# Kernel tuning notes

Hardware: AMD Instinct MI355X
Metric: run time of the kernel (lower is better)

The kernel has to match this reference:

```python
import jax, jax.numpy as jnp
import numpy as np

K_BITS = 8
QMAX = float(2 ** (K_BITS - 1) - 1)  # 127 for symmetric int8 fake quant
BN_EPS = 1e-5
RES_SCALE = 1.0


def _ste(v, q):
    # straight-through estimator: forward q, backward identity wrt v
    return v + jax.lax.stop_gradient(q - v)


def quant_act(x, alpha):
    # PAMS-style: clamp to learnable alpha, symmetric uniform fake-quant
    xc = jnp.clip(x, -alpha, alpha)
    scale = alpha / QMAX
    q = jnp.round(xc / scale) * scale
    return _ste(xc, q)


def quant_weight(w):
    # symmetric max-abs weight fake-quant
    scale = jnp.max(jnp.abs(w)) / QMAX
    q = jnp.clip(jnp.round(w / scale), -QMAX, QMAX) * scale
    return _ste(w, q)


def conv3x3(x, w):
    return jax.lax.conv_general_dilated(
        x, w, window_strides=(1, 1), padding=[(1, 1), (1, 1)],
        dimension_numbers=("NCHW", "OIHW", "NCHW"))


def batchnorm(x, gamma, beta):
    # training-mode BN: biased batch statistics over (N, H, W)
    mean = jnp.mean(x, axis=(0, 2, 3), keepdims=True)
    var = jnp.var(x, axis=(0, 2, 3), keepdims=True)
    xhat = (x - mean) * jax.lax.rsqrt(var + BN_EPS)
    return xhat * gamma[None, :, None, None] + beta[None, :, None, None]


def prelu(x, a):
    return jnp.where(x >= 0, x, a * x)


def setup_inputs() -> dict:
    key = jax.random.key(0)
    ks = jax.random.split(key, 4)
    C = 64
    identity = jax.random.normal(ks[0], (8, C, 192, 192), dtype=jnp.float32)
    # conv weights, default_init_weights scale 0.1 (kaiming-ish * 0.1)
    w1 = jax.random.normal(ks[1], (C, C, 3, 3), dtype=jnp.float32) * 0.1
    w2 = jax.random.normal(ks[2], (C, C, 3, 3), dtype=jnp.float32) * 0.1
    return {
        "identity": identity,
        "bits": jnp.ones((1,), jnp.float32),
        "f": jnp.ones((1,), jnp.float32),
        "bits_out": jnp.zeros((1,), jnp.float32),
        "w1": w1,
        "w2": w2,
        "alpha1": jnp.array(8.0, jnp.float32),
        "alpha2": jnp.array(8.0, jnp.float32),
        "gamma1": jnp.ones((C,), jnp.float32),
        "beta1": jnp.zeros((C,), jnp.float32),
        "gamma2": jnp.ones((C,), jnp.float32),
        "beta2": jnp.zeros((C,), jnp.float32),
        "prelu_a": jnp.array(0.25, jnp.float32),
        "shortcut": jnp.ones((1,), jnp.float32),
    }


def reference(identity, bits, f, bits_out, w1, w2, alpha1, alpha2,
              gamma1, beta1, gamma2, beta2, prelu_a, shortcut):
    # quant conv1: quantize input act + weights, 3x3 conv
    x = conv3x3(quant_act(identity, alpha1), quant_weight(w1))
    # PReLU then BN1 (module applies bn1(act(x)))
    x = batchnorm(prelu(x, prelu_a), gamma1, beta1)
    # quant conv2
    out = conv3x3(quant_act(x, alpha2), quant_weight(w2))
    out = batchnorm(out, gamma2, beta2)
    out = identity * shortcut + out * RES_SCALE
    return (out, bits, f, bits_out)
```

## Files before the change

kernel.cpp:

```cpp
#include <hip/hip_runtime.h>
#include <hip/hip_bf16.h>
#include <math.h>

#define CNUM   64
#define HH     192
#define WW     192
#define NBATCH 8
#define HWSZ   (HH * WW)
#define CHWSZ  (CNUM * HWSZ)
#define TOTALSZ ((size_t)NBATCH * CHWSZ)
#define QMAXF  127.0f
#define BNEPS  1e-5f
#define PW     194

typedef __attribute__((ext_vector_type(8))) short bf16x8;
typedef __attribute__((ext_vector_type(4))) float f32x4;

#define OFF_PK1    0
#define OFF_PK2    18432
#define OFF_STATS  36864
#define OFF_SUM1   36864
#define OFF_SSQ1   37120
#define OFF_SUM2   37376
#define OFF_SSQ2   37632
#define OFF_WMAX   37888
#define OFF_SW     37890
#define OFF_QA     38148
#define OFF_QB     (38148 + 9634816)

__device__ inline void gload16(const void* g, void* l) {
    __builtin_amdgcn_global_load_lds(
        (const __attribute__((address_space(1))) unsigned int*)g,
        (__attribute__((address_space(3))) unsigned int*)l, 16, 0, 0);
}
__device__ inline float bf2f(unsigned short u) {
    return __builtin_bit_cast(float, (unsigned)u << 16);
}

__global__ __launch_bounds__(256)
void wmax_kernel(const float* __restrict__ w1,
                 const float* __restrict__ w2,
                 unsigned* __restrict__ wmaxbits) {
    const int which = blockIdx.y;
    const float4* w4 = (const float4*)(which ? w2 : w1);
    const int b = (blockIdx.x * 256 + threadIdx.x) * 2;
    const float4 a = w4[b], c = w4[b + 1];
    float m = fmaxf(fmaxf(fmaxf(fabsf(a.x), fabsf(a.y)), fmaxf(fabsf(a.z), fabsf(a.w))),
                    fmaxf(fmaxf(fabsf(c.x), fabsf(c.y)), fmaxf(fabsf(c.z), fabsf(c.w))));
#pragma unroll
    for (int off = 1; off < 64; off <<= 1) m = fmaxf(m, __shfl_xor(m, off));
    if ((threadIdx.x & 63) == 0)
        atomicMax(wmaxbits + which, __builtin_bit_cast(unsigned, m));
}

__global__ __launch_bounds__(256)
void wpack_kernel(const float* __restrict__ w1,
                  const float* __restrict__ w2,
                  const unsigned* __restrict__ wmaxbits,
                  short* __restrict__ pk1,
                  short* __restrict__ pk2,
                  float* __restrict__ swout) {
    const int which = blockIdx.y;
    const float* w  = which ? w2 : w1;
    short*       pk = which ? pk2 : pk1;
    const float scale = __builtin_bit_cast(float, wmaxbits[which]) / QMAXF;
    if (blockIdx.x == 0 && threadIdx.x == 0) swout[which] = scale;
    const int i0 = (blockIdx.x * 256 + threadIdx.x) * 8;
#pragma unroll
    for (int k = 0; k < 8; ++k) {
        const int i = i0 + k;
        const int j   = i & 7;
        const int l   = (i >> 3) & 63;
        const int ocb = (i >> 9) & 3;
        const int icb = (i >> 11) & 1;
        const int t   = i >> 12;
        const int oc  = ocb * 16 + (l & 15);
        const int ic  = icb * 32 + ((l >> 4) & 3) * 8 + j;
        float q = rintf(w[oc * 576 + ic * 9 + t] / scale);
        q = fminf(fmaxf(q, -QMAXF), QMAXF);
        pk[i] = (short)(__builtin_bit_cast(unsigned, q) >> 16);
    }
}

__global__ __launch_bounds__(256)
void requant_kernel(const float* __restrict__ inp,
                    const float* __restrict__ alpha_p,
                    short* __restrict__ q) {
    const int tid  = threadIdx.x;
    const int xblk = blockIdx.x;
    const int py   = blockIdx.y;
    const int n    = blockIdx.z;
    short* qrow = q + ((size_t)n * PW + py) * (PW * 64);

    if (py == 0 || py == PW - 1) {
        for (int i = xblk * 256 + tid; i < PW * 64 * 2 / 16; i += 768)
            ((int4*)qrow)[i] = make_int4(0, 0, 0, 0);
        return;
    }
    if (xblk == 0 && tid < 8) ((int4*)qrow)[tid] = make_int4(0, 0, 0, 0);
    if (xblk == 2 && tid < 8) ((int4*)(qrow + 193 * 64))[tid] = make_int4(0, 0, 0, 0);

    const int gy = py - 1;
    const int x0 = xblk * 64;
    const float alpha  = alpha_p[0];
    const float inv_qs = QMAXF / alpha;

    __shared__ short s[64 * 72];
    const int xq  = tid & 15;
    const int icl = tid >> 4;

    float4 r[4];
#pragma unroll
    for (int p = 0; p < 4; ++p) {
        const int ic = icl * 4 + p;
        const size_t fo = ((size_t)n * CNUM + ic) * HWSZ + (size_t)gy * WW + x0 + xq * 4;
        r[p] = *(const float4*)(inp + fo);
    }
#pragma unroll
    for (int p = 0; p < 4; ++p) {
        const int ic = icl * 4 + p;
        float vv[4] = {r[p].x, r[p].y, r[p].z, r[p].w};
#pragma unroll
        for (int j = 0; j < 4; ++j) {
            float v = fminf(fmaxf(vv[j], -alpha), alpha);
            v = rintf(v * inv_qs);
            s[(xq * 4 + j) * 72 + ic] = (short)(__builtin_bit_cast(unsigned, v) >> 16);
        }
    }
    __syncthreads();
#pragma unroll
    for (int h = 0; h < 2; ++h) {
        const int t    = h * 256 + tid;
        const int xx   = t >> 3;
        const int slot = t & 7;
        const int px   = 1 + xblk * 64 + xx;
        const int g    = slot ^ (px & 7);
        const int4 val = *(const int4*)&s[xx * 72 + g * 8];
        *(int4*)(qrow + (size_t)px * 64 + slot * 8) = val;
    }
}

template<int XFORM, int SWZOUT>
__global__ __launch_bounds__(256, 3)
void conv_mfma_kernel(const short* __restrict__ q,
                      const short* __restrict__ wpk,
                      const float* __restrict__ swp,
                      const float* __restrict__ alpha_p,
                      const float* __restrict__ slope_p,
                      const float* __restrict__ st_sum,
                      const float* __restrict__ st_ssq,
                      const float* __restrict__ st_gamma,
                      const float* __restrict__ st_beta,
                      unsigned short* __restrict__ outp,
                      short* __restrict__ out_swz,
                      float* __restrict__ sum_g,
                      float* __restrict__ ssq_g) {
    __shared__ short s_in[6 * 66 * 64];
    __shared__ float sred[4 * 64], ssred[4 * 64];
    __shared__ float sab[128];

    const int tid = threadIdx.x;
    const int x0 = blockIdx.x * 64;
    const int y0 = blockIdx.y * 4;
    const int n  = blockIdx.z;
    const short* g0 = q + ((size_t)(n * PW + y0) * PW + x0) * 64;

    if (XFORM) {
        if (tid < 64) {
            const float cnt = (float)(NBATCH * HWSZ);
            const float sm = st_sum[tid] + st_sum[64 + tid] + st_sum[128 + tid] + st_sum[192 + tid];
            const float sq = st_ssq[tid] + st_ssq[64 + tid] + st_ssq[128 + tid] + st_ssq[192 + tid];
            const float mean = sm / cnt;
            const float var  = sq / cnt - mean * mean;
            const float inv  = 1.0f / sqrtf(var + BNEPS);
            const float a = st_gamma[tid] * inv;
            sab[tid] = a;
            sab[64 + tid] = st_beta[tid] - mean * a;
        }
        __syncthreads();
        const float alpha  = alpha_p[0];
        const float inv_qs = QMAXF / alpha;
#pragma unroll
        for (int k = 0; k < 13; ++k) {
            const int c = tid + k * 256;
            if (k == 12 && c >= 3168) break;
            const int r  = c / 528;
            const int w  = c - r * 528;
            const int pxl = w >> 3, slot = w & 7;
            const int px = x0 + pxl, py = y0 + r;
            int4 val = make_int4(0, 0, 0, 0);
            if ((unsigned)(px - 1) < 192u && (unsigned)(py - 1) < 192u) {
                const int4 v = *(const int4*)(g0 + (size_t)r * (PW * 64) + w * 8);
                const unsigned short* u = (const unsigned short*)&v;
                const int gch = slot ^ (px & 7);
                const float4 a0 = *(const float4*)&sab[gch * 8];
                const float4 a1 = *(const float4*)&sab[gch * 8 + 4];
                const float4 b0 = *(const float4*)&sab[64 + gch * 8];
                const float4 b1 = *(const float4*)&sab[64 + gch * 8 + 4];
                const float av[8] = {a0.x, a0.y, a0.z, a0.w, a1.x, a1.y, a1.z, a1.w};
                const float bv[8] = {b0.x, b0.y, b0.z, b0.w, b1.x, b1.y, b1.z, b1.w};
                unsigned wv[4];
#pragma unroll
                for (int jj = 0; jj < 4; ++jj) {
                    float xx0 = av[jj * 2]     * bf2f(u[jj * 2])     + bv[jj * 2];
                    float xx1 = av[jj * 2 + 1] * bf2f(u[jj * 2 + 1]) + bv[jj * 2 + 1];
                    xx0 = fminf(fmaxf(xx0, -alpha), alpha);
                    xx1 = fminf(fmaxf(xx1, -alpha), alpha);
                    xx0 = rintf(xx0 * inv_qs);
                    xx1 = rintf(xx1 * inv_qs);
                    wv[jj] = (__builtin_bit_cast(unsigned, xx1) & 0xffff0000u) |
                             (__builtin_bit_cast(unsigned, xx0) >> 16);
                }
                val = make_int4((int)wv[0], (int)wv[1], (int)wv[2], (int)wv[3]);
            }
            *(int4*)&s_in[c * 8] = val;
        }
    } else {
        for (int c = tid; c < 3168; c += 256) {
            const int r = c / 528;
            const int w = c - r * 528;
            gload16(g0 + (size_t)r * (PW * 64) + w * 8, &s_in[c * 8]);
        }
    }
    __syncthreads();

    const int wave  = tid >> 6;
    const int lane  = tid & 63;
    const int xlane = lane & 15;
    const int icgl  = lane >> 4;

    f32x4 acc[4][4];
#pragma unroll
    for (int m = 0; m < 4; ++m)
#pragma unroll
        for (int nb = 0; nb < 4; ++nb) acc[m][nb] = (f32x4){0.f, 0.f, 0.f, 0.f};

#pragma unroll
    for (int t = 0; t < 9; ++t) {
        const int ky = t / 3, kx = t % 3;
        const int r = wave + ky;
#pragma unroll
        for (int icb = 0; icb < 2; ++icb) {
            const int icg = icb * 4 + icgl;
            bf16x8 bfrag[4], afrag[4];
            const short* bp = wpk + (size_t)((t * 2 + icb) * 4) * 512 + lane * 8;
#pragma unroll
            for (int nb = 0; nb < 4; ++nb) bfrag[nb] = *(const bf16x8*)(bp + nb * 512);
#pragma unroll
            for (int m = 0; m < 4; ++m) {
                const int x = m * 16 + xlane + kx;
                afrag[m] = *(const bf16x8*)&s_in[(size_t)((r * 66 + x) * 8 + (icg ^ (x & 7))) * 8];
            }
#pragma unroll
            for (int m = 0; m < 4; ++m)
#pragma unroll
                for (int nb = 0; nb < 4; ++nb)
                    acc[m][nb] = __builtin_amdgcn_mfma_f32_16x16x32_bf16(
                        afrag[m], bfrag[nb], acc[m][nb], 0, 0, 0);
        }
    }

    const float sfin  = (alpha_p[0] / QMAXF) * swp[0];
    const float slope = slope_p ? slope_p[0] : 1.0f;
    const int gy  = y0 + wave;
    const int gx0 = x0 + icgl * 4;

    if (SWZOUT) __syncthreads();
    short* sT = s_in + wave * (64 * 72);

#pragma unroll
    for (int nb = 0; nb < 4; ++nb) {
        const int oc = nb * 16 + xlane;
        float s = 0.0f, ss = 0.0f;
#pragma unroll
        for (int m = 0; m < 4; ++m) {
            float v[4];
#pragma unroll
            for (int rgi = 0; rgi < 4; ++rgi) {
                float a = acc[m][nb][rgi] * sfin;
                a = (a >= 0.0f) ? a : slope * a;
                v[rgi] = a;
                s += a;
                ss += a * a;
            }
            if (SWZOUT) {
#pragma unroll
                for (int rgi = 0; rgi < 4; ++rgi) {
                    const int pxl = m * 16 + icgl * 4 + rgi;
                    sT[pxl * 72 + oc] = (short)__builtin_bit_cast(
                        unsigned short, __float2bfloat16(v[rgi]));
                }
            } else {
                ushort4 pk;
                pk.x = __builtin_bit_cast(unsigned short, __float2bfloat16(v[0]));
                pk.y = __builtin_bit_cast(unsigned short, __float2bfloat16(v[1]));
                pk.z = __builtin_bit_cast(unsigned short, __float2bfloat16(v[2]));
                pk.w = __builtin_bit_cast(unsigned short, __float2bfloat16(v[3]));
                *(ushort4*)&outp[(size_t)(n * CNUM + oc) * HWSZ + (size_t)gy * WW + gx0 + m * 16] = pk;
            }
        }
        s  += __shfl_xor(s, 16);  s  += __shfl_xor(s, 32);
        ss += __shfl_xor(ss, 16); ss += __shfl_xor(ss, 32);
        if (icgl == 0) { sred[wave * 64 + oc] = s; ssred[wave * 64 + oc] = ss; }
    }

    if (SWZOUT) {
        const int py = gy + 1;
        short* qrow = out_swz + ((size_t)n * PW + py) * (PW * 64);
#pragma unroll
        for (int k = 0; k < 8; ++k) {
            const int idx  = k * 64 + lane;
            const int xx   = idx >> 3;
            const int slot = idx & 7;
            const int px   = x0 + 1 + xx;
            const int g    = slot ^ (px & 7);
            *(int4*)(qrow + (size_t)px * 64 + slot * 8) = *(const int4*)&sT[xx * 72 + g * 8];
        }
    }

    __syncthreads();
    const int bank = (blockIdx.y ^ blockIdx.z) & 3;
    if (tid < 64) {
        atomicAdd(sum_g + bank * 64 + tid,
                  sred[tid] + sred[64 + tid] + sred[128 + tid] + sred[192 + tid]);
    } else if (tid < 128) {
        const int c = tid - 64;
        atomicAdd(ssq_g + bank * 64 + c,
                  ssred[c] + ssred[64 + c] + ssred[128 + c] + ssred[192 + c]);
    }
}

__global__ __launch_bounds__(256)
void final_kernel(const float* __restrict__ identity,
                  const unsigned short* __restrict__ t2,
                  const float* __restrict__ st_sum,
                  const float* __restrict__ st_ssq,
                  const float* __restrict__ st_gamma,
                  const float* __restrict__ st_beta,
                  const float* __restrict__ shortcut_p,
                  const float* __restrict__ bits,
                  const float* __restrict__ f,
                  const float* __restrict__ bits_out,
                  float* __restrict__ out) {
    __shared__ float sab[128];
    if (threadIdx.x < 64) {
        const int c = threadIdx.x;
        const float cnt = (float)(NBATCH * HWSZ);
        const float sm = st_sum[c] + st_sum[64 + c] + st_sum[128 + c] + st_sum[192 + c];
        const float sq = st_ssq[c] + st_ssq[64 + c] + st_ssq[128 + c] + st_ssq[192 + c];
        const float mean = sm / cnt;
        const float var  = sq / cnt - mean * mean;
        const float inv  = 1.0f / sqrtf(var + BNEPS);
        const float a = st_gamma[c] * inv;
        sab[c] = a;
        sab[64 + c] = st_beta[c] - mean * a;
    }
    __syncthreads();

    const size_t base = (size_t)blockIdx.x * 1024;
    const int   cch  = (int)((base / (HWSZ / 4)) % CNUM);
    const float a  = sab[cch];
    const float bb = sab[64 + cch];
    const float sc = shortcut_p[0];

    float4  idv[4];
    ushort4 tv[4];
#pragma unroll
    for (int k = 0; k < 4; ++k) {
        const size_t i4 = base + (size_t)k * 256 + threadIdx.x;
        idv[k] = ((const float4*)identity)[i4];
        tv[k]  = ((const ushort4*)t2)[i4];
    }
#pragma unroll
    for (int k = 0; k < 4; ++k) {
        const size_t i4 = base + (size_t)k * 256 + threadIdx.x;
        float4 o;
        o.x = idv[k].x * sc + a * bf2f(tv[k].x) + bb;
        o.y = idv[k].y * sc + a * bf2f(tv[k].y) + bb;
        o.z = idv[k].z * sc + a * bf2f(tv[k].z) + bb;
        o.w = idv[k].w * sc + a * bf2f(tv[k].w) + bb;
        ((float4*)out)[i4] = o;
    }
    if (blockIdx.x == 0 && threadIdx.x == 0) {
        out[TOTALSZ + 0] = bits[0];
        out[TOTALSZ + 1] = f[0];
        out[TOTALSZ + 2] = bits_out[0];
    }
}

extern "C" void kernel_launch(void* const* d_in, const int* in_sizes, int n_in,
                              void* d_out, int out_size, void* d_ws, size_t ws_size,
                              hipStream_t stream) {
    const float* identity = (const float*)d_in[0];
    const float* bits     = (const float*)d_in[1];
    const float* f        = (const float*)d_in[2];
    const float* bits_out = (const float*)d_in[3];
    const float* w1       = (const float*)d_in[4];
    const float* w2       = (const float*)d_in[5];
    const float* alpha1   = (const float*)d_in[6];
    const float* alpha2   = (const float*)d_in[7];
    const float* gamma1   = (const float*)d_in[8];
    const float* beta1    = (const float*)d_in[9];
    const float* gamma2   = (const float*)d_in[10];
    const float* beta2    = (const float*)d_in[11];
    const float* prelu_a  = (const float*)d_in[12];
    const float* shortcut = (const float*)d_in[13];
    float* out = (float*)d_out;
    float* ws  = (float*)d_ws;

    short*    pk1   = (short*)(ws + OFF_PK1);
    short*    pk2   = (short*)(ws + OFF_PK2);
    float*    sum1  = ws + OFF_SUM1;
    float*    ssq1  = ws + OFF_SSQ1;
    float*    sum2  = ws + OFF_SUM2;
    float*    ssq2  = ws + OFF_SSQ2;
    unsigned* wmaxb = (unsigned*)(ws + OFF_WMAX);
    float*    sw    = ws + OFF_SW;
    short*          qa = (short*)(ws + OFF_QA);
    short*          qb = (short*)(ws + OFF_QB);
    unsigned short* t2 = (unsigned short*)(ws + OFF_QA);

    hipMemsetAsync(ws + OFF_STATS, 0, 1026 * sizeof(float), stream);
    hipLaunchKernelGGL(wmax_kernel, dim3(18, 2), dim3(256), 0, stream, w1, w2, wmaxb);
    hipLaunchKernelGGL(requant_kernel, dim3(3, PW, NBATCH), dim3(256), 0, stream,
                       identity, alpha1, qa);
    hipLaunchKernelGGL(wpack_kernel, dim3(18, 2), dim3(256), 0, stream,
                       w1, w2, wmaxb, pk1, pk2, sw);
    hipLaunchKernelGGL((conv_mfma_kernel<0, 1>), dim3(3, HH / 4, NBATCH), dim3(256), 0, stream,
                       qa, pk1, sw + 0, alpha1, prelu_a,
                       (const float*)nullptr, (const float*)nullptr,
                       (const float*)nullptr, (const float*)nullptr,
                       (unsigned short*)nullptr, qb, sum1, ssq1);
    hipLaunchKernelGGL((conv_mfma_kernel<1, 0>), dim3(3, HH / 4, NBATCH), dim3(256), 0, stream,
                       qb, pk2, sw + 1, alpha2, (const float*)nullptr,
                       sum1, ssq1, gamma1, beta1,
                       t2, (short*)nullptr, sum2, ssq2);
    hipLaunchKernelGGL(final_kernel, dim3((unsigned)(TOTALSZ / 4 / 1024)), dim3(256), 0, stream,
                       identity, t2, sum2, ssq2, gamma2, beta2,
                       shortcut, bits, f, bits_out, out);
}
```

Before: 268.0 us.

## Make conv kernels persistent with double-buffered LDS tile prefetch and 512-thread blocks

Both conv passes now launch a fixed grid of 256 persistent blocks. Each block walks the tiles in a strided loop and prefetches the next tile's input into a second LDS buffer while the MFMA loop runs on the current one. Blocks grow to 8 waves, each owning one output row and half the output channels. BN statistics are accumulated in registers across tiles and flushed with one atomic per wave at the end, which cuts per-tile reduction and atomic traffic. In exchange the kernel uses much more LDS and fewer blocks fit per CU, and only 256 blocks may underfill the GPU's CUs.

```diff
diff --git a/kernel.cpp b/kernel.cpp
--- a/kernel.cpp
+++ b/kernel.cpp
@@ -12,6 +12,8 @@
 #define QMAXF  127.0f
 #define BNEPS  1e-5f
 #define PW     194
+#define NTILES (3 * 48 * NBATCH)
+#define NBLK   256
 
 typedef __attribute__((ext_vector_type(8))) short bf16x8;
 typedef __attribute__((ext_vector_type(4))) float f32x4;
@@ -35,6 +37,14 @@
 }
 __device__ inline float bf2f(unsigned short u) {
     return __builtin_bit_cast(float, (unsigned)u << 16);
+}
+__device__ inline void tdec(int T, int& x0, int& y0, int& n) {
+    const int xt = T % 3;
+    const int r  = T / 3;
+    const int yt = r % 48;
+    n  = r / 48;
+    x0 = xt * 64;
+    y0 = yt * 4;
 }
 
 __global__ __launch_bounds__(256)
@@ -141,7 +151,7 @@
 }
 
 template<int XFORM, int SWZOUT>
-__global__ __launch_bounds__(256, 3)
+__global__ __launch_bounds__(512, 2)
 void conv_mfma_kernel(const short* __restrict__ q,
                       const short* __restrict__ wpk,
                       const float* __restrict__ swp,
@@ -155,15 +165,22 @@
                       short* __restrict__ out_swz,
                       float* __restrict__ sum_g,
                       float* __restrict__ ssq_g) {
-    __shared__ short s_in[6 * 66 * 64];
-    __shared__ float sred[4 * 64], ssred[4 * 64];
+    __shared__ short s_in[2][6 * 66 * 64];
+    __shared__ short sT[SWZOUT ? 4 * 64 * 72 : 64];
     __shared__ float sab[128];
 
-    const int tid = threadIdx.x;
-    const int x0 = blockIdx.x * 64;
-    const int y0 = blockIdx.y * 4;
-    const int n  = blockIdx.z;
-    const short* g0 = q + ((size_t)(n * PW + y0) * PW + x0) * 64;
+    const int tid   = threadIdx.x;
+    const int wave  = tid >> 6;
+    const int lane  = tid & 63;
+    const int xlane = lane & 15;
+    const int icgl  = lane >> 4;
+    const int row   = wave >> 1;
+    const int nbh   = wave & 1;
+
+    const float alpha  = alpha_p[0];
+    const float inv_qs = QMAXF / alpha;
+    const float sfin   = (alpha / QMAXF) * swp[0];
+    const float slope  = slope_p ? slope_p[0] : 1.0f;
 
     if (XFORM) {
         if (tid < 64) {
@@ -178,155 +195,224 @@
             sab[64 + tid] = st_beta[tid] - mean * a;
         }
         __syncthreads();
-        const float alpha  = alpha_p[0];
-        const float inv_qs = QMAXF / alpha;
-#pragma unroll
-        for (int k = 0; k < 13; ++k) {
-            const int c = tid + k * 256;
-            if (k == 12 && c >= 3168) break;
-            const int r  = c / 528;
-            const int w  = c - r * 528;
-            const int pxl = w >> 3, slot = w & 7;
-            const int px = x0 + pxl, py = y0 + r;
-            int4 val = make_int4(0, 0, 0, 0);
-            if ((unsigned)(px - 1) < 192u && (unsigned)(py - 1) < 192u) {
-                const int4 v = *(const int4*)(g0 + (size_t)r * (PW * 64) + w * 8);
-                const unsigned short* u = (const unsigned short*)&v;
-                const int gch = slot ^ (px & 7);
-                const float4 a0 = *(const float4*)&sab[gch * 8];
-                const float4 a1 = *(const float4*)&sab[gch * 8 + 4];
-                const float4 b0 = *(const float4*)&sab[64 + gch * 8];
-                const float4 b1 = *(const float4*)&sab[64 + gch * 8 + 4];
-                const float av[8] = {a0.x, a0.y, a0.z, a0.w, a1.x, a1.y, a1.z, a1.w};
-                const float bv[8] = {b0.x, b0.y, b0.z, b0.w, b1.x, b1.y, b1.z, b1.w};
-                unsigned wv[4];
-#pragma unroll
-                for (int jj = 0; jj < 4; ++jj) {
-                    float xx0 = av[jj * 2]     * bf2f(u[jj * 2])     + bv[jj * 2];
-                    float xx1 = av[jj * 2 + 1] * bf2f(u[jj * 2 + 1]) + bv[jj * 2 + 1];
-                    xx0 = fminf(fmaxf(xx0, -alpha), alpha);
-                    xx1 = fminf(fmaxf(xx1, -alpha), alpha);
-                    xx0 = rintf(xx0 * inv_qs);
-                    xx1 = rintf(xx1 * inv_qs);
-                    wv[jj] = (__builtin_bit_cast(unsigned, xx1) & 0xffff0000u) |
-                             (__builtin_bit_cast(unsigned, xx0) >> 16);
-                }
-                val = make_int4((int)wv[0], (int)wv[1], (int)wv[2], (int)wv[3]);
-            }
-            *(int4*)&s_in[c * 8] = val;
-        }
-    } else {
-        for (int c = tid; c < 3168; c += 256) {
-            const int r = c / 528;
-            const int w = c - r * 528;
-            gload16(g0 + (size_t)r * (PW * 64) + w * 8, &s_in[c * 8]);
+    }
+
+    float st_s[2]  = {0.f, 0.f};
+    float st_ss[2] = {0.f, 0.f};
+
+    {
+        int x0, y0, n;
+        tdec(blockIdx.x, x0, y0, n);
+        const short* g0 = q + ((size_t)(n * PW + y0) * PW + x0) * 64;
+        if (!XFORM) {
+            for (int c = tid; c < 3168; c += 512) {
+                const int r = c / 528;
+                const int w = c - r * 528;
+                gload16(g0 + (size_t)r * (PW * 64) + w * 8, &s_in[0][c * 8]);
+            }
+        } else {
+#pragma unroll
+            for (int k = 0; k < 7; ++k) {
+                const int c = tid + k * 512;
+                if (c < 3168) {
+                    const int r  = c / 528;
+                    const int w  = c - r * 528;
+                    const int pxl = w >> 3, slot = w & 7;
+                    const int px = x0 + pxl, py = y0 + r;
+                    int4 val = make_int4(0, 0, 0, 0);
+                    if ((unsigned)(px - 1) < 192u && (unsigned)(py - 1) < 192u) {
+                        const int4 v = *(const int4*)(g0 + (size_t)r * (PW * 64) + w * 8);
+                        const unsigned short* u = (const unsigned short*)&v;
+                        const int gch = slot ^ (px & 7);
+                        const float av[8] = {sab[gch*8+0], sab[gch*8+1], sab[gch*8+2], sab[gch*8+3],
+                                             sab[gch*8+4], sab[gch*8+5], sab[gch*8+6], sab[gch*8+7]};
+                        const float bv[8] = {sab[64+gch*8+0], sab[64+gch*8+1], sab[64+gch*8+2], sab[64+gch*8+3],
+                                             sab[64+gch*8+4], sab[64+gch*8+5], sab[64+gch*8+6], sab[64+gch*8+7]};
+                        unsigned wv[4];
+#pragma unroll
+                        for (int jj = 0; jj < 4; ++jj) {
+                            float xx0 = av[jj*2]   * bf2f(u[jj*2])   + bv[jj*2];
+                            float xx1 = av[jj*2+1] * bf2f(u[jj*2+1]) + bv[jj*2+1];
+                            xx0 = fminf(fmaxf(xx0, -alpha), alpha);
+                            xx1 = fminf(fmaxf(xx1, -alpha), alpha);
+                            xx0 = rintf(xx0 * inv_qs);
+                            xx1 = rintf(xx1 * inv_qs);
+                            wv[jj] = (__builtin_bit_cast(unsigned, xx1) & 0xffff0000u) |
+                                     (__builtin_bit_cast(unsigned, xx0) >> 16);
+                        }
+                        val = make_int4((int)wv[0], (int)wv[1], (int)wv[2], (int)wv[3]);
+                    }
+                    *(int4*)&s_in[0][c * 8] = val;
+                }
+            }
         }
     }
     __syncthreads();
 
-    const int wave  = tid >> 6;
-    const int lane  = tid & 63;
-    const int xlane = lane & 15;
-    const int icgl  = lane >> 4;
-
-    f32x4 acc[4][4];
-#pragma unroll
-    for (int m = 0; m < 4; ++m)
-#pragma unroll
-        for (int nb = 0; nb < 4; ++nb) acc[m][nb] = (f32x4){0.f, 0.f, 0.f, 0.f};
-
-#pragma unroll
-    for (int t = 0; t < 9; ++t) {
-        const int ky = t / 3, kx = t % 3;
-        const int r = wave + ky;
-#pragma unroll
-        for (int icb = 0; icb < 2; ++icb) {
-            const int icg = icb * 4 + icgl;
-            bf16x8 bfrag[4], afrag[4];
-            const short* bp = wpk + (size_t)((t * 2 + icb) * 4) * 512 + lane * 8;
-#pragma unroll
-            for (int nb = 0; nb < 4; ++nb) bfrag[nb] = *(const bf16x8*)(bp + nb * 512);
+    int cur = 0;
+    for (int T = blockIdx.x; T < NTILES; T += NBLK) {
+        int x0, y0, n;
+        tdec(T, x0, y0, n);
+        const int  Tn = T + NBLK;
+        const bool hn = (Tn < NTILES);
+        int nx0 = 0, ny0 = 0, nn2 = 0;
+        if (hn) tdec(Tn, nx0, ny0, nn2);
+
+        int4 rg[7];
+        if (hn) {
+            const short* gn = q + ((size_t)(nn2 * PW + ny0) * PW + nx0) * 64;
+            if (!XFORM) {
+                for (int c = tid; c < 3168; c += 512) {
+                    const int r = c / 528;
+                    const int w = c - r * 528;
+                    gload16(gn + (size_t)r * (PW * 64) + w * 8, &s_in[cur ^ 1][c * 8]);
+                }
+            } else {
+#pragma unroll
+                for (int k = 0; k < 7; ++k) {
+                    const int c = tid + k * 512;
+                    if (c < 3168) {
+                        const int r = c / 528;
+                        const int w = c - r * 528;
+                        rg[k] = *(const int4*)(gn + (size_t)r * (PW * 64) + w * 8);
+                    }
+                }
+            }
+        }
+
+        const short* sbase = s_in[cur];
+        f32x4 acc[4][2];
+#pragma unroll
+        for (int m = 0; m < 4; ++m)
+#pragma unroll
+            for (int j = 0; j < 2; ++j) acc[m][j] = (f32x4){0.f, 0.f, 0.f, 0.f};
+
+#pragma unroll
+        for (int t = 0; t < 9; ++t) {
+            const int ky = t / 3, kx = t % 3;
+            const int r = row + ky;
+#pragma unroll
+            for (int icb = 0; icb < 2; ++icb) {
+                const int icg = icb * 4 + icgl;
+                bf16x8 bfrag[2], afrag[4];
+                const short* bp = wpk + (size_t)((t * 2 + icb) * 4 + nbh * 2) * 512 + lane * 8;
+                bfrag[0] = *(const bf16x8*)(bp);
+                bfrag[1] = *(const bf16x8*)(bp + 512);
+#pragma unroll
+                for (int m = 0; m < 4; ++m) {
+                    const int x = m * 16 + xlane + kx;
+                    afrag[m] = *(const bf16x8*)&sbase[(size_t)((r * 66 + x) * 8 + (icg ^ (x & 7))) * 8];
+                }
+#pragma unroll
+                for (int m = 0; m < 4; ++m)
+#pragma unroll
+                    for (int j = 0; j < 2; ++j)
+                        acc[m][j] = __builtin_amdgcn_mfma_f32_16x16x32_bf16(
+                            afrag[m], bfrag[j], acc[m][j], 0, 0, 0);
+            }
+        }
+
+        if (XFORM && hn) {
+#pragma unroll
+            for (int k = 0; k < 7; ++k) {
+                const int c = tid + k * 512;
+                if (c < 3168) {
+                    const int r = c / 528;
+                    const int w = c - r * 528;
+                    const int pxl = w >> 3, slot = w & 7;
+                    const int px = nx0 + pxl, py = ny0 + r;
+                    int4 val = make_int4(0, 0, 0, 0);
+                    if ((unsigned)(px - 1) < 192u && (unsigned)(py - 1) < 192u) {
+                        const unsigned short* u = (const unsigned short*)&rg[k];
+                        const int gch = slot ^ (px & 7);
+                        const float av[8] = {sab[gch*8+0], sab[gch*8+1], sab[gch*8+2], sab[gch*8+3],
+                                             sab[gch*8+4], sab[gch*8+5], sab[gch*8+6], sab[gch*8+7]};
+                        const float bv[8] = {sab[64+gch*8+0], sab[64+gch*8+1], sab[64+gch*8+2], sab[64+gch*8+3],
+                                             sab[64+gch*8+4], sab[64+gch*8+5], sab[64+gch*8+6], sab[64+gch*8+7]};
+                        unsigned wv[4];
+#pragma unroll
+                        for (int jj = 0; jj < 4; ++jj) {
+                            float xx0 = av[jj*2]   * bf2f(u[jj*2])   + bv[jj*2];
+                            float xx1 = av[jj*2+1] * bf2f(u[jj*2+1]) + bv[jj*2+1];
+                            xx0 = fminf(fmaxf(xx0, -alpha), alpha);
+                            xx1 = fminf(fmaxf(xx1, -alpha), alpha);
+                            xx0 = rintf(xx0 * inv_qs);
+                            xx1 = rintf(xx1 * inv_qs);
+                            wv[jj] = (__builtin_bit_cast(unsigned, xx1) & 0xffff0000u) |
+                                     (__builtin_bit_cast(unsigned, xx0) >> 16);
+                        }
+                        val = make_int4((int)wv[0], (int)wv[1], (int)wv[2], (int)wv[3]);
+                    }
+                    *(int4*)&s_in[cur ^ 1][c * 8] = val;
+                }
+            }
+        }
+
+        const int gy  = y0 + row;
+        const int gx0 = x0 + icgl * 4;
+#pragma unroll
+        for (int nb2 = 0; nb2 < 2; ++nb2) {
+            const int oc = nbh * 32 + nb2 * 16 + xlane;
 #pragma unroll
             for (int m = 0; m < 4; ++m) {
-                const int x = m * 16 + xlane + kx;
-                afrag[m] = *(const bf16x8*)&s_in[(size_t)((r * 66 + x) * 8 + (icg ^ (x & 7))) * 8];
-            }
-#pragma unroll
-            for (int m = 0; m < 4; ++m)
-#pragma unroll
-                for (int nb = 0; nb < 4; ++nb)
-                    acc[m][nb] = __builtin_amdgcn_mfma_f32_16x16x32_bf16(
-                        afrag[m], bfrag[nb], acc[m][nb], 0, 0, 0);
-        }
-    }
-
-    const float sfin  = (alpha_p[0] / QMAXF) * swp[0];
-    const float slope = slope_p ? slope_p[0] : 1.0f;
-    const int gy  = y0 + wave;
-    const int gx0 = x0 + icgl * 4;
-
-    if (SWZOUT) __syncthreads();
-    short* sT = s_in + wave * (64 * 72);
-
-#pragma unroll
-    for (int nb = 0; nb < 4; ++nb) {
-        const int oc = nb * 16 + xlane;
-        float s = 0.0f, ss = 0.0f;
-#pragma unroll
-        for (int m = 0; m < 4; ++m) {
-            float v[4];
-#pragma unroll
-            for (int rgi = 0; rgi < 4; ++rgi) {
-                float a = acc[m][nb][rgi] * sfin;
-                a = (a >= 0.0f) ? a : slope * a;
-                v[rgi] = a;
-                s += a;
-                ss += a * a;
-            }
-            if (SWZOUT) {
+                float v[4];
 #pragma unroll
                 for (int rgi = 0; rgi < 4; ++rgi) {
-                    const int pxl = m * 16 + icgl * 4 + rgi;
-                    sT[pxl * 72 + oc] = (short)__builtin_bit_cast(
-                        unsigned short, __float2bfloat16(v[rgi]));
-                }
-            } else {
-                ushort4 pk;
-                pk.x = __builtin_bit_cast(unsigned short, __float2bfloat16(v[0]));
-                pk.y = __builtin_bit_cast(unsigned short, __float2bfloat16(v[1]));
-                pk.z = __builtin_bit_cast(unsigned short, __float2bfloat16(v[2]));
-                pk.w = __builtin_bit_cast(unsigned short, __float2bfloat16(v[3]));
-                *(ushort4*)&outp[(size_t)(n * CNUM + oc) * HWSZ + (size_t)gy * WW + gx0 + m * 16] = pk;
-            }
-        }
+                    float a = acc[m][nb2][rgi] * sfin;
+                    a = (a >= 0.0f) ? a : slope * a;
+                    v[rgi] = a;
+                    st_s[nb2]  += a;
+                    st_ss[nb2] += a * a;
+                }
+                if (SWZOUT) {
+#pragma unroll
+                    for (int rgi = 0; rgi < 4; ++rgi) {
+                        const int pxl = m * 16 + icgl * 4 + rgi;
+                        sT[row * (64 * 72) + pxl * 72 + oc] = (short)__builtin_bit_cast(
+                            unsigned short, __float2bfloat16(v[rgi]));
+                    }
+                } else {
+                    ushort4 pk;
+                    pk.x = __builtin_bit_cast(unsigned short, __float2bfloat16(v[0]));
+                    pk.y = __builtin_bit_cast(unsigned short, __float2bfloat16(v[1]));
+                    pk.z = __builtin_bit_cast(unsigned short, __float2bfloat16(v[2]));
+                    pk.w = __builtin_bit_cast(unsigned short, __float2bfloat16(v[3]));
+                    *(ushort4*)&outp[(size_t)(n * CNUM + oc) * HWSZ + (size_t)gy * WW + gx0 + m * 16] = pk;
+                }
+            }
+        }
+
+        __syncthreads();
+
+        if (SWZOUT) {
+            const int py = gy + 1;
+            short* qrow = out_swz + ((size_t)n * PW + py) * (PW * 64);
+#pragma unroll
+            for (int kk = 0; kk < 4; ++kk) {
+                const int idx  = (nbh * 4 + kk) * 64 + lane;
+                const int xx   = idx >> 3;
+                const int slot = idx & 7;
+                const int px   = x0 + 1 + xx;
+                const int g    = slot ^ (px & 7);
+                *(int4*)(qrow + (size_t)px * 64 + slot * 8) =
+                    *(const int4*)&sT[row * (64 * 72) + xx * 72 + g * 8];
+            }
+            __syncthreads();
+        }
+        cur ^= 1;
+    }
+
+#pragma unroll
+    for (int nb2 = 0; nb2 < 2; ++nb2) {
+        float s = st_s[nb2], ss = st_ss[nb2];
         s  += __shfl_xor(s, 16);  s  += __shfl_xor(s, 32);
         ss += __shfl_xor(ss, 16); ss += __shfl_xor(ss, 32);
-        if (icgl == 0) { sred[wave * 64 + oc] = s; ssred[wave * 64 + oc] = ss; }
-    }
-
-    if (SWZOUT) {
-        const int py = gy + 1;
-        short* qrow = out_swz + ((size_t)n * PW + py) * (PW * 64);
-#pragma unroll
-        for (int k = 0; k < 8; ++k) {
-            const int idx  = k * 64 + lane;
-            const int xx   = idx >> 3;
-            const int slot = idx & 7;
-            const int px   = x0 + 1 + xx;
-            const int g    = slot ^ (px & 7);
-            *(int4*)(qrow + (size_t)px * 64 + slot * 8) = *(const int4*)&sT[xx * 72 + g * 8];
-        }
-    }
-
-    __syncthreads();
-    const int bank = (blockIdx.y ^ blockIdx.z) & 3;
-    if (tid < 64) {
-        atomicAdd(sum_g + bank * 64 + tid,
-                  sred[tid] + sred[64 + tid] + sred[128 + tid] + sred[192 + tid]);
-    } else if (tid < 128) {
-        const int c = tid - 64;
-        atomicAdd(ssq_g + bank * 64 + c,
-                  ssred[c] + ssred[64 + c] + ssred[128 + c] + ssred[192 + c]);
+        if (icgl == 0) {
+            const int oc   = nbh * 32 + nb2 * 16 + xlane;
+            const int bank = wave & 3;
+            atomicAdd(sum_g + bank * 64 + oc, s);
+            atomicAdd(ssq_g + bank * 64 + oc, ss);
+        }
     }
 }
 
@@ -426,12 +512,12 @@
                        identity, alpha1, qa);
     hipLaunchKernelGGL(wpack_kernel, dim3(18, 2), dim3(256), 0, stream,
                        w1, w2, wmaxb, pk1, pk2, sw);
-    hipLaunchKernelGGL((conv_mfma_kernel<0, 1>), dim3(3, HH / 4, NBATCH), dim3(256), 0, stream,
+    hipLaunchKernelGGL((conv_mfma_kernel<0, 1>), dim3(NBLK), dim3(512), 0, stream,
                        qa, pk1, sw + 0, alpha1, prelu_a,
                        (const float*)nullptr, (const float*)nullptr,
                        (const float*)nullptr, (const float*)nullptr,
                        (unsigned short*)nullptr, qb, sum1, ssq1);
-    hipLaunchKernelGGL((conv_mfma_kernel<1, 0>), dim3(3, HH / 4, NBATCH), dim3(256), 0, stream,
+    hipLaunchKernelGGL((conv_mfma_kernel<1, 0>), dim3(NBLK), dim3(512), 0, stream,
                        qb, pk2, sw + 1, alpha2, (const float*)nullptr,
                        sum1, ssq1, gamma1, beta1,
                        t2, (short*)nullptr, sum2, ssq2);
```

Result: slower. 366.7 us (+36.8%).

## Switch conv MFMA from bf16 to int8 with new packed layouts

Applied to the files above, without the earlier changes.

Stores the quantized activations and weights as int8 instead of bf16-encoded integers and uses the i32 16x16x64 int8 MFMA, which halves the number of matrix instructions and halves LDS and global traffic for the conv1 input. This is exact because the values are integers in [-127,127] and accumulate in int32. It brings new swizzle layouts for the padded activation buffer, weight packing and LDS staging. The conv1 epilogue now transposes through a separate LDS buffer in two halves with extra barriers. The intermediate between the convs stays bf16 and is requantized to int8 while being loaded.

```diff
diff --git a/kernel.cpp b/kernel.cpp
--- a/kernel.cpp
+++ b/kernel.cpp
@@ -13,8 +13,7 @@
 #define BNEPS  1e-5f
 #define PW     194
 
-typedef __attribute__((ext_vector_type(8))) short bf16x8;
-typedef __attribute__((ext_vector_type(4))) float f32x4;
+typedef __attribute__((ext_vector_type(4))) int i32x4;
 
 #define OFF_PK1    0
 #define OFF_PK2    18432
@@ -57,48 +56,47 @@
 void wpack_kernel(const float* __restrict__ w1,
                   const float* __restrict__ w2,
                   const unsigned* __restrict__ wmaxbits,
-                  short* __restrict__ pk1,
-                  short* __restrict__ pk2,
+                  char* __restrict__ pk1,
+                  char* __restrict__ pk2,
                   float* __restrict__ swout) {
     const int which = blockIdx.y;
     const float* w  = which ? w2 : w1;
-    short*       pk = which ? pk2 : pk1;
+    char*        pk = which ? pk2 : pk1;
     const float scale = __builtin_bit_cast(float, wmaxbits[which]) / QMAXF;
     if (blockIdx.x == 0 && threadIdx.x == 0) swout[which] = scale;
     const int i0 = (blockIdx.x * 256 + threadIdx.x) * 8;
 #pragma unroll
     for (int k = 0; k < 8; ++k) {
         const int i = i0 + k;
-        const int j   = i & 7;
-        const int l   = (i >> 3) & 63;
-        const int ocb = (i >> 9) & 3;
-        const int icb = (i >> 11) & 1;
+        const int j   = i & 15;
+        const int l   = (i >> 4) & 63;
+        const int ocb = (i >> 10) & 3;
         const int t   = i >> 12;
         const int oc  = ocb * 16 + (l & 15);
-        const int ic  = icb * 32 + ((l >> 4) & 3) * 8 + j;
+        const int ic  = ((l >> 4) & 3) * 16 + j;
         float q = rintf(w[oc * 576 + ic * 9 + t] / scale);
         q = fminf(fmaxf(q, -QMAXF), QMAXF);
-        pk[i] = (short)(__builtin_bit_cast(unsigned, q) >> 16);
+        pk[i] = (char)(int)q;
     }
 }
 
 __global__ __launch_bounds__(256)
 void requant_kernel(const float* __restrict__ inp,
                     const float* __restrict__ alpha_p,
-                    short* __restrict__ q) {
+                    char* __restrict__ q) {
     const int tid  = threadIdx.x;
     const int xblk = blockIdx.x;
     const int py   = blockIdx.y;
     const int n    = blockIdx.z;
-    short* qrow = q + ((size_t)n * PW + py) * (PW * 64);
+    char* qrow = q + ((size_t)n * PW + py) * (PW * 64);
 
     if (py == 0 || py == PW - 1) {
-        for (int i = xblk * 256 + tid; i < PW * 64 * 2 / 16; i += 768)
+        for (int i = xblk * 256 + tid; i < PW * 4; i += 768)
             ((int4*)qrow)[i] = make_int4(0, 0, 0, 0);
         return;
     }
-    if (xblk == 0 && tid < 8) ((int4*)qrow)[tid] = make_int4(0, 0, 0, 0);
-    if (xblk == 2 && tid < 8) ((int4*)(qrow + 193 * 64))[tid] = make_int4(0, 0, 0, 0);
+    if (xblk == 0 && tid < 4) ((int4*)qrow)[tid] = make_int4(0, 0, 0, 0);
+    if (xblk == 2 && tid < 4) ((int4*)(qrow + 193 * 64))[tid] = make_int4(0, 0, 0, 0);
 
     const int gy = py - 1;
     const int x0 = xblk * 64;
@@ -124,26 +122,28 @@
         for (int j = 0; j < 4; ++j) {
             float v = fminf(fmaxf(vv[j], -alpha), alpha);
             v = rintf(v * inv_qs);
-            s[(xq * 4 + j) * 72 + ic] = (short)(__builtin_bit_cast(unsigned, v) >> 16);
+            s[(xq * 4 + j) * 72 + ic] = (short)(int)v;
         }
     }
     __syncthreads();
-#pragma unroll
-    for (int h = 0; h < 2; ++h) {
-        const int t    = h * 256 + tid;
-        const int xx   = t >> 3;
-        const int slot = t & 7;
-        const int px   = 1 + xblk * 64 + xx;
-        const int g    = slot ^ (px & 7);
-        const int4 val = *(const int4*)&s[xx * 72 + g * 8];
-        *(int4*)(qrow + (size_t)px * 64 + slot * 8) = val;
+    {
+        const int xx = tid >> 2;
+        const int g  = tid & 3;
+        const int px = 1 + x0 + xx;
+        const int gp = g ^ ((px >> 1) & 3);
+        const short* sp = &s[xx * 72 + g * 16];
+        int4 val;
+        char* vb = (char*)&val;
+#pragma unroll
+        for (int j = 0; j < 16; ++j) vb[j] = (char)sp[j];
+        *(int4*)(qrow + (size_t)px * 64 + gp * 16) = val;
     }
 }
 
 template<int XFORM, int SWZOUT>
 __global__ __launch_bounds__(256, 3)
-void conv_mfma_kernel(const short* __restrict__ q,
-                      const short* __restrict__ wpk,
+void conv_mfma_kernel(const char* __restrict__ q,
+                      const char* __restrict__ wpk,
                       const float* __restrict__ swp,
                       const float* __restrict__ alpha_p,
                       const float* __restrict__ slope_p,
@@ -152,18 +152,21 @@
                       const float* __restrict__ st_gamma,
                       const float* __restrict__ st_beta,
                       unsigned short* __restrict__ outp,
-                      short* __restrict__ out_swz,
+                      unsigned short* __restrict__ out_swz,
                       float* __restrict__ sum_g,
                       float* __restrict__ ssq_g) {
-    __shared__ short s_in[6 * 66 * 64];
-    __shared__ float sred[4 * 64], ssred[4 * 64];
+    __shared__ __align__(16) char s_in[1584 * 16];
+    __shared__ __align__(16) short sT[SWZOUT ? 4 * 64 * 40 : 8];
+    __shared__ float sred[256], ssred[256];
     __shared__ float sab[128];
 
     const int tid = threadIdx.x;
     const int x0 = blockIdx.x * 64;
     const int y0 = blockIdx.y * 4;
     const int n  = blockIdx.z;
-    const short* g0 = q + ((size_t)(n * PW + y0) * PW + x0) * 64;
+
+    const float alpha  = alpha_p[0];
+    const float inv_qs = QMAXF / alpha;
 
     if (XFORM) {
         if (tid < 64) {
@@ -178,48 +181,51 @@
             sab[64 + tid] = st_beta[tid] - mean * a;
         }
         __syncthreads();
-        const float alpha  = alpha_p[0];
-        const float inv_qs = QMAXF / alpha;
-#pragma unroll
-        for (int k = 0; k < 13; ++k) {
+        const unsigned short* qv = (const unsigned short*)q;
+        const unsigned short* qb0 = qv + ((size_t)(n * PW + y0) * PW + x0) * 64;
+#pragma unroll
+        for (int k = 0; k < 7; ++k) {
             const int c = tid + k * 256;
-            if (k == 12 && c >= 3168) break;
-            const int r  = c / 528;
-            const int w  = c - r * 528;
-            const int pxl = w >> 3, slot = w & 7;
-            const int px = x0 + pxl, py = y0 + r;
-            int4 val = make_int4(0, 0, 0, 0);
-            if ((unsigned)(px - 1) < 192u && (unsigned)(py - 1) < 192u) {
-                const int4 v = *(const int4*)(g0 + (size_t)r * (PW * 64) + w * 8);
-                const unsigned short* u = (const unsigned short*)&v;
-                const int gch = slot ^ (px & 7);
-                const float4 a0 = *(const float4*)&sab[gch * 8];
-                const float4 a1 = *(const float4*)&sab[gch * 8 + 4];
-                const float4 b0 = *(const float4*)&sab[64 + gch * 8];
-                const float4 b1 = *(const float4*)&sab[64 + gch * 8 + 4];
-                const float av[8] = {a0.x, a0.y, a0.z, a0.w, a1.x, a1.y, a1.z, a1.w};
-                const float bv[8] = {b0.x, b0.y, b0.z, b0.w, b1.x, b1.y, b1.z, b1.w};
-                unsigned wv[4];
-#pragma unroll
-                for (int jj = 0; jj < 4; ++jj) {
-                    float xx0 = av[jj * 2]     * bf2f(u[jj * 2])     + bv[jj * 2];
-                    float xx1 = av[jj * 2 + 1] * bf2f(u[jj * 2 + 1]) + bv[jj * 2 + 1];
-                    xx0 = fminf(fmaxf(xx0, -alpha), alpha);
-                    xx1 = fminf(fmaxf(xx1, -alpha), alpha);
-                    xx0 = rintf(xx0 * inv_qs);
-                    xx1 = rintf(xx1 * inv_qs);
-                    wv[jj] = (__builtin_bit_cast(unsigned, xx1) & 0xffff0000u) |
-                             (__builtin_bit_cast(unsigned, xx0) >> 16);
+            if (c < 1584) {
+                const int r  = c / 264;
+                const int w  = c - r * 264;
+                const int x  = w >> 2, gp = w & 3;
+                const int px = x0 + x, pyy = y0 + r;
+                int4 val = make_int4(0, 0, 0, 0);
+                if ((unsigned)(px - 1) < 192u && (unsigned)(pyy - 1) < 192u) {
+                    const int g16 = gp ^ ((x >> 1) & 3);
+                    const unsigned short* qp = qb0 + (size_t)r * (PW * 64) + (size_t)x * 64;
+                    const int s0 = (2 * g16) ^ (px & 7);
+                    const int4 v0 = *(const int4*)(qp + s0 * 8);
+                    const int4 v1 = *(const int4*)(qp + (s0 ^ 1) * 8);
+                    const unsigned short* u0 = (const unsigned short*)&v0;
+                    const unsigned short* u1 = (const unsigned short*)&v1;
+                    char vb[16];
+#pragma unroll
+                    for (int jj = 0; jj < 8; ++jj) {
+                        const int ic = g16 * 16 + jj;
+                        float xx0 = sab[ic] * bf2f(u0[jj]) + sab[64 + ic];
+                        xx0 = fminf(fmaxf(xx0, -alpha), alpha);
+                        vb[jj] = (char)(int)rintf(xx0 * inv_qs);
+                    }
+#pragma unroll
+                    for (int jj = 0; jj < 8; ++jj) {
+                        const int ic = g16 * 16 + 8 + jj;
+                        float xx1 = sab[ic] * bf2f(u1[jj]) + sab[64 + ic];
+                        xx1 = fminf(fmaxf(xx1, -alpha), alpha);
+                        vb[8 + jj] = (char)(int)rintf(xx1 * inv_qs);
+                    }
+                    val = *(int4*)vb;
                 }
-                val = make_int4((int)wv[0], (int)wv[1], (int)wv[2], (int)wv[3]);
+                *(int4*)&s_in[c * 16] = val;
             }
-            *(int4*)&s_in[c * 8] = val;
         }
     } else {
-        for (int c = tid; c < 3168; c += 256) {
-            const int r = c / 528;
-            const int w = c - r * 528;
-            gload16(g0 + (size_t)r * (PW * 64) + w * 8, &s_in[c * 8]);
+        const char* g0 = q + ((size_t)(n * PW + y0) * PW + x0) * 64;
+        for (int c = tid; c < 1584; c += 256) {
+            const int r = c / 264;
+            const int w = c - r * 264;
+            gload16(g0 + (size_t)r * (PW * 64) + w * 16, &s_in[c * 16]);
         }
     }
     __syncthreads();
@@ -229,68 +235,97 @@
     const int xlane = lane & 15;
     const int icgl  = lane >> 4;
 
-    f32x4 acc[4][4];
+    i32x4 acc[4][4];
 #pragma unroll
     for (int m = 0; m < 4; ++m)
 #pragma unroll
-        for (int nb = 0; nb < 4; ++nb) acc[m][nb] = (f32x4){0.f, 0.f, 0.f, 0.f};
+        for (int nb = 0; nb < 4; ++nb) acc[m][nb] = (i32x4){0, 0, 0, 0};
 
 #pragma unroll
     for (int t = 0; t < 9; ++t) {
         const int ky = t / 3, kx = t % 3;
         const int r = wave + ky;
-#pragma unroll
-        for (int icb = 0; icb < 2; ++icb) {
-            const int icg = icb * 4 + icgl;
-            bf16x8 bfrag[4], afrag[4];
-            const short* bp = wpk + (size_t)((t * 2 + icb) * 4) * 512 + lane * 8;
-#pragma unroll
-            for (int nb = 0; nb < 4; ++nb) bfrag[nb] = *(const bf16x8*)(bp + nb * 512);
-#pragma unroll
-            for (int m = 0; m < 4; ++m) {
-                const int x = m * 16 + xlane + kx;
-                afrag[m] = *(const bf16x8*)&s_in[(size_t)((r * 66 + x) * 8 + (icg ^ (x & 7))) * 8];
-            }
-#pragma unroll
-            for (int m = 0; m < 4; ++m)
-#pragma unroll
-                for (int nb = 0; nb < 4; ++nb)
-                    acc[m][nb] = __builtin_amdgcn_mfma_f32_16x16x32_bf16(
-                        afrag[m], bfrag[nb], acc[m][nb], 0, 0, 0);
-        }
-    }
-
-    const float sfin  = (alpha_p[0] / QMAXF) * swp[0];
+        i32x4 bfrag[4], afrag[4];
+        const char* bp = wpk + ((size_t)(t * 4) * 64 + lane) * 16;
+#pragma unroll
+        for (int nb = 0; nb < 4; ++nb) bfrag[nb] = *(const i32x4*)(bp + (size_t)nb * 1024);
+#pragma unroll
+        for (int m = 0; m < 4; ++m) {
+            const int x = m * 16 + xlane + kx;
+            afrag[m] = *(const i32x4*)&s_in[(size_t)((r * 66 + x) * 4 + (icgl ^ ((x >> 1) & 3))) * 16];
+        }
+#pragma unroll
+        for (int m = 0; m < 4; ++m)
+#pragma unroll
+            for (int nb = 0; nb < 4; ++nb)
+                acc[m][nb] = __builtin_amdgcn_mfma_i32_16x16x64_i8(
+                    afrag[m], bfrag[nb], acc[m][nb], 0, 0, 0);
+    }
+
+    const float sfin  = (alpha / QMAXF) * swp[0];
     const float slope = slope_p ? slope_p[0] : 1.0f;
     const int gy  = y0 + wave;
     const int gx0 = x0 + icgl * 4;
 
-    if (SWZOUT) __syncthreads();
-    short* sT = s_in + wave * (64 * 72);
-
-#pragma unroll
-    for (int nb = 0; nb < 4; ++nb) {
-        const int oc = nb * 16 + xlane;
-        float s = 0.0f, ss = 0.0f;
-#pragma unroll
-        for (int m = 0; m < 4; ++m) {
-            float v[4];
-#pragma unroll
-            for (int rgi = 0; rgi < 4; ++rgi) {
-                float a = acc[m][nb][rgi] * sfin;
-                a = (a >= 0.0f) ? a : slope * a;
-                v[rgi] = a;
-                s += a;
-                ss += a * a;
+    if (SWZOUT) {
+#pragma unroll
+        for (int h = 0; h < 2; ++h) {
+#pragma unroll
+            for (int nbi = 0; nbi < 2; ++nbi) {
+                const int nb = 2 * h + nbi;
+                const int oc = nb * 16 + xlane;
+                float s = 0.0f, ss = 0.0f;
+#pragma unroll
+                for (int m = 0; m < 4; ++m) {
+#pragma unroll
+                    for (int rgi = 0; rgi < 4; ++rgi) {
+                        float a = (float)acc[m][nb][rgi] * sfin;
+                        a = (a >= 0.0f) ? a : slope * a;
+                        s += a;
+                        ss += a * a;
+                        const int pxl = m * 16 + icgl * 4 + rgi;
+                        sT[(wave * 64 + pxl) * 40 + (nbi * 16 + xlane)] =
+                            (short)__builtin_bit_cast(unsigned short, __float2bfloat16(a));
+                    }
+                }
+                s  += __shfl_xor(s, 16);  s  += __shfl_xor(s, 32);
+                ss += __shfl_xor(ss, 16); ss += __shfl_xor(ss, 32);
+                if (icgl == 0) { sred[wave * 64 + oc] = s; ssred[wave * 64 + oc] = ss; }
             }
-            if (SWZOUT) {
+            __syncthreads();
+            {
+                const int py = gy + 1;
+                unsigned short* qrow = out_swz + ((size_t)n * PW + py) * (PW * 64);
+#pragma unroll
+                for (int kk = 0; kk < 4; ++kk) {
+                    const int idx = kk * 64 + lane;
+                    const int xx  = idx >> 2;
+                    const int gg  = idx & 3;
+                    const int g8  = h * 4 + gg;
+                    const int px  = x0 + 1 + xx;
+                    const int slot = g8 ^ (px & 7);
+                    *(int4*)(qrow + (size_t)px * 64 + slot * 8) =
+                        *(const int4*)&sT[(wave * 64 + xx) * 40 + gg * 8];
+                }
+            }
+            __syncthreads();
+        }
+    } else {
+#pragma unroll
+        for (int nb = 0; nb < 4; ++nb) {
+            const int oc = nb * 16 + xlane;
+            float s = 0.0f, ss = 0.0f;
+#pragma unroll
+            for (int m = 0; m < 4; ++m) {
+                float v[4];
 #pragma unroll
                 for (int rgi = 0; rgi < 4; ++rgi) {
-                    const int pxl = m * 16 + icgl * 4 + rgi;
-                    sT[pxl * 72 + oc] = (short)__builtin_bit_cast(
-                        unsigned short, __float2bfloat16(v[rgi]));
+                    float a = (float)acc[m][nb][rgi] * sfin;
+                    a = (a >= 0.0f) ? a : slope * a;
+                    v[rgi] = a;
+                    s += a;
+                    ss += a * a;
                 }
-            } else {
                 ushort4 pk;
                 pk.x = __builtin_bit_cast(unsigned short, __float2bfloat16(v[0]));
                 pk.y = __builtin_bit_cast(unsigned short, __float2bfloat16(v[1]));
@@ -298,27 +333,13 @@
                 pk.w = __builtin_bit_cast(unsigned short, __float2bfloat16(v[3]));
                 *(ushort4*)&outp[(size_t)(n * CNUM + oc) * HWSZ + (size_t)gy * WW + gx0 + m * 16] = pk;
             }
-        }
-        s  += __shfl_xor(s, 16);  s  += __shfl_xor(s, 32);
-        ss += __shfl_xor(ss, 16); ss += __shfl_xor(ss, 32);
-        if (icgl == 0) { sred[wave * 64 + oc] = s; ssred[wave * 64 + oc] = ss; }
-    }
-
-    if (SWZOUT) {
-        const int py = gy + 1;
-        short* qrow = out_swz + ((size_t)n * PW + py) * (PW * 64);
-#pragma unroll
-        for (int k = 0; k < 8; ++k) {
-            const int idx  = k * 64 + lane;
-            const int xx   = idx >> 3;
-            const int slot = idx & 7;
-            const int px   = x0 + 1 + xx;
-            const int g    = slot ^ (px & 7);
-            *(int4*)(qrow + (size_t)px * 64 + slot * 8) = *(const int4*)&sT[xx * 72 + g * 8];
-        }
-    }
-
-    __syncthreads();
+            s  += __shfl_xor(s, 16);  s  += __shfl_xor(s, 32);
+            ss += __shfl_xor(ss, 16); ss += __shfl_xor(ss, 32);
+            if (icgl == 0) { sred[wave * 64 + oc] = s; ssred[wave * 64 + oc] = ss; }
+        }
+        __syncthreads();
+    }
+
     const int bank = (blockIdx.y ^ blockIdx.z) & 3;
     if (tid < 64) {
         atomicAdd(sum_g + bank * 64 + tid,
@@ -408,16 +429,16 @@
     float* out = (float*)d_out;
     float* ws  = (float*)d_ws;
 
-    short*    pk1   = (short*)(ws + OFF_PK1);
-    short*    pk2   = (short*)(ws + OFF_PK2);
+    char*     pk1   = (char*)(ws + OFF_PK1);
+    char*     pk2   = (char*)(ws + OFF_PK2);
     float*    sum1  = ws + OFF_SUM1;
     float*    ssq1  = ws + OFF_SSQ1;
     float*    sum2  = ws + OFF_SUM2;
     float*    ssq2  = ws + OFF_SSQ2;
     unsigned* wmaxb = (unsigned*)(ws + OFF_WMAX);
     float*    sw    = ws + OFF_SW;
-    short*          qa = (short*)(ws + OFF_QA);
-    short*          qb = (short*)(ws + OFF_QB);
+    char*           qa = (char*)(ws + OFF_QA);
+    unsigned short* qb = (unsigned short*)(ws + OFF_QB);
     unsigned short* t2 = (unsigned short*)(ws + OFF_QA);
 
     hipMemsetAsync(ws + OFF_STATS, 0, 1026 * sizeof(float), stream);
@@ -432,9 +453,9 @@
                        (const float*)nullptr, (const float*)nullptr,
                        (unsigned short*)nullptr, qb, sum1, ssq1);
     hipLaunchKernelGGL((conv_mfma_kernel<1, 0>), dim3(3, HH / 4, NBATCH), dim3(256), 0, stream,
-                       qb, pk2, sw + 1, alpha2, (const float*)nullptr,
+                       (const char*)qb, pk2, sw + 1, alpha2, (const float*)nullptr,
                        sum1, ssq1, gamma1, beta1,
-                       t2, (short*)nullptr, sum2, ssq2);
+                       t2, (unsigned short*)nullptr, sum2, ssq2);
     hipLaunchKernelGGL(final_kernel, dim3((unsigned)(TOTALSZ / 4 / 1024)), dim3(256), 0, stream,
                        identity, t2, sum2, ssq2, gamma2, beta2,
                        shortcut, bits, f, bits_out, out);
```

Result: faster. 250.9 us, median of 2 (-6.4%).
